# Optimization experiments

Hardware: AMD Instinct MI355X
Metric: run time of the kernel (lower is better)

The kernel has to match this reference:

```python
import jax, jax.numpy as jnp
import numpy as np

NUM_GROUPS = 4
KERNEL_SIZE = 3


def _conv1x1(x, w, b):
    # x: [B,Cin,H,W], w: [Cout,Cin], b: [Cout]
    return jnp.einsum('bchw,oc->bohw', x, w) + b[None, :, None, None]


def _unfold(t, ks):
    # t: [B,G,Gd,H,W] -> patches [B,G,Gd,ks*ks,H,W] with zero padding (pad=ks//2)
    pad = ks // 2
    H, W = t.shape[-2:]
    tp = jnp.pad(t, ((0, 0), (0, 0), (0, 0), (pad, pad), (pad, pad)))
    return jnp.stack([tp[..., i:i + H, j:j + W]
                      for i in range(ks) for j in range(ks)], axis=3)


def setup_inputs() -> dict:
    key = jax.random.key(0)
    ks = jax.random.split(key, 7)
    B, Cin, C, H, W = 4, 256, 256, 64, 64
    s = 1.0 / np.sqrt(Cin)
    return {
        'x': jax.random.normal(ks[0], (B, Cin, H, W), dtype=jnp.float32),
        'wq': jax.random.normal(ks[1], (C, Cin), dtype=jnp.float32) * s,
        'bq': jax.random.normal(ks[2], (C,), dtype=jnp.float32) * 0.01,
        'wk': jax.random.normal(ks[3], (C, Cin), dtype=jnp.float32) * s,
        'bk': jax.random.normal(ks[4], (C,), dtype=jnp.float32) * 0.01,
        'wv': jax.random.normal(ks[5], (C, Cin), dtype=jnp.float32) * s,
        'bv': jax.random.normal(ks[6], (C,), dtype=jnp.float32) * 0.01,
    }


def reference(x, wq, bq, wk, bk, wv, bv):
    B, _, H, W = x.shape
    C = wq.shape[0]
    G = NUM_GROUPS
    Gd = C // G
    q = _conv1x1(x, wq, bq).reshape(B, G, Gd, H, W)
    k = _conv1x1(x, wk, bk).reshape(B, G, Gd, H, W)
    v = _conv1x1(x, wv, bv).reshape(B, G, Gd, H, W)
    kp = _unfold(k, KERNEL_SIZE)  # [B,G,Gd,k2,H,W]
    vp = _unfold(v, KERNEL_SIZE)  # [B,G,Gd,k2,H,W]
    attn = jnp.einsum('bgdhw,bgdphw->bgphw', q, kp)  # [B,G,k2,H,W]
    attn = jax.nn.softmax(attn, axis=2)
    out = jnp.einsum('bgphw,bgdphw->bgdhw', attn, vp)  # [B,G,Gd,H,W]
    return out.reshape(B, C, H, W)
```

## Files before the change

kernel.cpp:

```cpp
#include <hip/hip_runtime.h>
#include <cstddef>
#include <cstdint>

#define BDIM 4
#define HH   64
#define WW   64
#define NG   4
#define GD   64
#define HWSZ 4096
#define NTOT 16384
#define CIN  256

typedef __attribute__((ext_vector_type(4))) float f32x4;
typedef _Float16 f16x4_t __attribute__((ext_vector_type(4)));
typedef _Float16 f16x8_t __attribute__((ext_vector_type(8)));

__device__ __forceinline__ void lds_load16(const void* g, void* l) {
    __builtin_amdgcn_global_load_lds(
        (const __attribute__((address_space(1))) unsigned int*)g,
        (__attribute__((address_space(3))) unsigned int*)l, 16, 0, 0);
}

__global__ __launch_bounds__(256) void qkv_gemm_kernel(
    const float* __restrict__ x,
    const float* __restrict__ wq, const float* __restrict__ bq,
    const float* __restrict__ wk, const float* __restrict__ bk,
    const float* __restrict__ wv, const float* __restrict__ bv,
    _Float16* __restrict__ qh, _Float16* __restrict__ kh,
    _Float16* __restrict__ vh)
{
    __shared__ float As[128 * 32];
    __shared__ float Bs[32 * 128];

    const int t  = threadIdx.x;
    const int bx = blockIdx.x;
    const int u  = (bx & 7) * 96 + (bx >> 3);
    const int mt = u % 6;
    const int nt = u / 6;

    const int l     = t & 63;
    const int wid   = t >> 6;
    const int wm    = wid >> 1, wn = wid & 1;
    const int lrow  = l & 15;
    const int grp   = l >> 4;
    const int lk8   = grp * 8;
    const int lrow4 = grp * 4;

    const float* wsel = (mt < 2) ? wq : (mt < 4) ? wk : wv;
    const float* bsel = (mt < 2) ? bq : (mt < 4) ? bk : bv;
    _Float16*    osel = (mt < 2) ? qh : (mt < 4) ? kh : vh;
    const int    mtl  = mt & 1;

    const int bi  = nt >> 5;
    const int px0 = (nt & 31) * 128;
    const float* xb = x + (size_t)bi * CIN * HWSZ + px0;

    f32x4 acc[4][4];
    #pragma unroll
    for (int mi = 0; mi < 4; ++mi) {
        const f32x4 bb = *(const f32x4*)&bsel[mtl * 128 + wm * 64 + mi * 16 + lrow4];
        #pragma unroll
        for (int ni = 0; ni < 4; ++ni) acc[mi][ni] = bb;
    }

    const float* asrc[4];
    const float* bsrc[4];
    #pragma unroll
    for (int i = 0; i < 4; ++i) {
        const int w16 = i * 256 + t;
        {
            const int m  = w16 >> 3;
            const int kb = w16 & 7;
            asrc[i] = wsel + (size_t)(mtl * 128 + m) * CIN + ((kb ^ (m & 7)) * 4);
        }
        {
            const int k   = w16 >> 5;
            const int pxb = w16 & 31;
            bsrc[i] = xb + (size_t)k * HWSZ + ((pxb ^ ((k >> 3) << 2)) * 4);
        }
    }

    for (int kt = 0; kt < 8; ++kt) {
        #pragma unroll
        for (int i = 0; i < 4; ++i) {
            lds_load16(asrc[i] + kt * 32, As + (i * 256 + t) * 4);
            lds_load16(bsrc[i] + (size_t)kt * 32 * HWSZ, Bs + (i * 256 + t) * 4);
        }
        __syncthreads();

        f16x8_t af[4];
        #pragma unroll
        for (int mi = 0; mi < 4; ++mi) {
            const int m  = wm * 64 + mi * 16 + lrow;
            const int s  = m & 7;
            const f32x4 a0 = *(const f32x4*)&As[m * 32 + ((grp * 2) ^ s) * 4];
            const f32x4 a1 = *(const f32x4*)&As[m * 32 + ((grp * 2 + 1) ^ s) * 4];
            f16x8_t f;
            #pragma unroll
            for (int j = 0; j < 4; ++j) { f[j] = (_Float16)a0[j]; f[4 + j] = (_Float16)a1[j]; }
            af[mi] = f;
        }

        f16x8_t bf[4];
        #pragma unroll
        for (int ni = 0; ni < 4; ++ni) {
            const int px   = wn * 64 + ni * 16 + lrow;
            const int base = ((px >> 2) ^ (grp << 2)) * 4 + (px & 3);
            f16x8_t f;
            #pragma unroll
            for (int j = 0; j < 8; ++j) f[j] = (_Float16)Bs[(lk8 + j) * 128 + base];
            bf[ni] = f;
        }

        #pragma unroll
        for (int mi = 0; mi < 4; ++mi)
            #pragma unroll
            for (int ni = 0; ni < 4; ++ni)
                acc[mi][ni] = __builtin_amdgcn_mfma_f32_16x16x32_f16(
                    af[mi], bf[ni], acc[mi][ni], 0, 0, 0);
        __syncthreads();
    }

    #pragma unroll
    for (int ni = 0; ni < 4; ++ni) {
        const size_t ng = (size_t)(nt * 128 + wn * 64 + ni * 16 + lrow);
        #pragma unroll
        for (int mi = 0; mi < 4; ++mi) {
            f16x4_t hv;
            #pragma unroll
            for (int j = 0; j < 4; ++j) hv[j] = (_Float16)acc[mi][ni][j];
            const int chunk = mtl * 8 + wm * 4 + mi;
            *(f16x4_t*)&osel[((size_t)chunk * NTOT + ng) * 16 + lrow4] = hv;
        }
    }
}

__global__ __launch_bounds__(256) void loc_attn_kernel(
    const _Float16* __restrict__ qh, const _Float16* __restrict__ kh,
    const _Float16* __restrict__ vh, float* __restrict__ out)
{
    const int t   = threadIdx.x;
    const int bx0 = blockIdx.x;
    const int bx  = (bx0 & 7) * 128 + (bx0 >> 3);
    const int h = bx & 63;
    const int g = (bx >> 6) & 3;
    const int b = bx >> 8;

    const int wl  = t & 15;
    const int c   = (t >> 4) & 3;
    const int wid = t >> 6;
    const int w   = wid * 16 + wl;

    const int ck = g * 4 + c;
    const size_t n = (size_t)b * HWSZ + h * 64 + w;

    float qf[16];
    {
        const _Float16* qp = &qh[((size_t)ck * NTOT + n) * 16];
        const f16x8_t q0 = *(const f16x8_t*)qp;
        const f16x8_t q1 = *(const f16x8_t*)(qp + 8);
        #pragma unroll
        for (int j = 0; j < 8; ++j) { qf[j] = (float)q0[j]; qf[8 + j] = (float)q1[j]; }
    }

    float logit[9];
    #pragma unroll
    for (int p = 0; p < 9; ++p) {
        const int dh = p / 3 - 1, dw = p % 3 - 1;
        const int hh = h + dh, ww2 = w + dw;
        float part = 0.f;
        if (hh >= 0 && hh < HH && ww2 >= 0 && ww2 < WW) {
            const size_t nn = (size_t)b * HWSZ + hh * 64 + ww2;
            const _Float16* kp = &kh[((size_t)ck * NTOT + nn) * 16];
            const f16x8_t k0 = *(const f16x8_t*)kp;
            const f16x8_t k1 = *(const f16x8_t*)(kp + 8);
            #pragma unroll
            for (int j = 0; j < 8; ++j)
                part += qf[j] * (float)k0[j] + qf[8 + j] * (float)k1[j];
        }
        part += __shfl_xor(part, 16, 64);
        part += __shfl_xor(part, 32, 64);
        logit[p] = part;
    }

    float mx = logit[0];
    #pragma unroll
    for (int p = 1; p < 9; ++p) mx = fmaxf(mx, logit[p]);
    float a[9];
    float s = 0.f;
    #pragma unroll
    for (int p = 0; p < 9; ++p) { a[p] = __expf(logit[p] - mx); s += a[p]; }
    const float inv = 1.f / s;
    #pragma unroll
    for (int p = 0; p < 9; ++p) a[p] *= inv;

    float acc[16];
    #pragma unroll
    for (int dd = 0; dd < 16; ++dd) acc[dd] = 0.f;
    #pragma unroll
    for (int p = 0; p < 9; ++p) {
        const int dh = p / 3 - 1, dw = p % 3 - 1;
        const int hh = h + dh, ww2 = w + dw;
        if (hh < 0 || hh >= HH || ww2 < 0 || ww2 >= WW) continue;
        const size_t nn = (size_t)b * HWSZ + hh * 64 + ww2;
        const _Float16* vp = &vh[((size_t)ck * NTOT + nn) * 16];
        const f16x8_t v0 = *(const f16x8_t*)vp;
        const f16x8_t v1 = *(const f16x8_t*)(vp + 8);
        const float ap = a[p];
        #pragma unroll
        for (int j = 0; j < 8; ++j) {
            acc[j]     += ap * (float)v0[j];
            acc[8 + j] += ap * (float)v1[j];
        }
    }

    const int obase = b * 256 + g * 64 + c * 16;
    const int off = h * 64 + w;
    #pragma unroll
    for (int dd = 0; dd < 16; ++dd)
        out[(size_t)(obase + dd) * HWSZ + off] = acc[dd];
}

extern "C" void kernel_launch(void* const* d_in, const int* in_sizes, int n_in,
                              void* d_out, int out_size, void* d_ws, size_t ws_size,
                              hipStream_t stream) {
    const float* x  = (const float*)d_in[0];
    const float* wq = (const float*)d_in[1];
    const float* bq = (const float*)d_in[2];
    const float* wk = (const float*)d_in[3];
    const float* bk = (const float*)d_in[4];
    const float* wv = (const float*)d_in[5];
    const float* bv = (const float*)d_in[6];
    float* out = (float*)d_out;

    char* ws = (char*)d_ws;
    _Float16* qh = (_Float16*)ws;
    _Float16* kh = (_Float16*)(ws + 8388608);
    _Float16* vh = (_Float16*)(ws + 16777216);

    qkv_gemm_kernel<<<dim3(768), 256, 0, stream>>>(x, wq, bq, wk, bk, wv, bv,
                                                   qh, kh, vh);
    loc_attn_kernel<<<dim3(1024), 256, 0, stream>>>(qh, kh, vh, out);
}
```

Measured before the change: 34.07 us.

## Fuse QKV projection and local attention into one kernel with halo recompute

Replaces the two-kernel pipeline (QKV GEMM writing fp16 workspace, then local attention reading it) with a single kernel per (batch, group, 4-row tile). Each block computes Q and K for its rows plus a one-row halo into LDS, runs the softmax, then computes V into LDS and accumulates the output. This removes the workspace round trip through global memory and one launch. In exchange it recomputes the halo rows (6 rows computed for 4 output rows), uses only 256 blocks of 512 threads, and needs large LDS, which may limit occupancy and parallelism.

```diff
diff --git a/kernel.cpp b/kernel.cpp
--- a/kernel.cpp
+++ b/kernel.cpp
@@ -5,10 +5,7 @@
 #define BDIM 4
 #define HH   64
 #define WW   64
-#define NG   4
-#define GD   64
 #define HWSZ 4096
-#define NTOT 16384
 #define CIN  256
 
 typedef __attribute__((ext_vector_type(4))) float f32x4;
@@ -21,204 +18,254 @@
         (__attribute__((address_space(3))) unsigned int*)l, 16, 0, 0);
 }
 
-__global__ __launch_bounds__(256) void qkv_gemm_kernel(
+__global__ __launch_bounds__(512, 2) void fused_kernel(
     const float* __restrict__ x,
     const float* __restrict__ wq, const float* __restrict__ bq,
     const float* __restrict__ wk, const float* __restrict__ bk,
     const float* __restrict__ wv, const float* __restrict__ bv,
-    _Float16* __restrict__ qh, _Float16* __restrict__ kh,
-    _Float16* __restrict__ vh)
+    float* __restrict__ out)
 {
-    __shared__ float As[128 * 32];
-    __shared__ float Bs[32 * 128];
-
-    const int t  = threadIdx.x;
-    const int bx = blockIdx.x;
-    const int u  = (bx & 7) * 96 + (bx >> 3);
-    const int mt = u % 6;
-    const int nt = u / 6;
-
-    const int l     = t & 63;
-    const int wid   = t >> 6;
-    const int wm    = wid >> 1, wn = wid & 1;
-    const int lrow  = l & 15;
-    const int grp   = l >> 4;
-    const int lk8   = grp * 8;
-    const int lrow4 = grp * 4;
-
-    const float* wsel = (mt < 2) ? wq : (mt < 4) ? wk : wv;
-    const float* bsel = (mt < 2) ? bq : (mt < 4) ? bk : bv;
-    _Float16*    osel = (mt < 2) ? qh : (mt < 4) ? kh : vh;
-    const int    mtl  = mt & 1;
-
-    const int bi  = nt >> 5;
-    const int px0 = (nt & 31) * 128;
-    const float* xb = x + (size_t)bi * CIN * HWSZ + px0;
-
-    f32x4 acc[4][4];
+    __shared__ float    As[128 * 32];
+    __shared__ float    Bs[32 * 384];
+    __shared__ _Float16 qlds[256 * 64];
+    __shared__ _Float16 klds[384 * 64];
+
+    const int t   = threadIdx.x;
+    const int bx0 = blockIdx.x;
+    const int bx  = (bx0 & 7) * 32 + (bx0 >> 3);
+    const int g   = bx & 3;
+    const int ht  = (bx >> 2) & 15;
+    const int b   = bx >> 6;
+    const int h0  = ht * 4;
+
+    const int l    = t & 63;
+    const int wid  = t >> 6;
+    const int lrow = l & 15;
+    const int grp  = l >> 4;
+    const int grp4 = grp * 4;
+    const int wmA  = wid >> 2;
+    const int wnA  = wid & 3;
+
+    const float* xb = x + (size_t)b * CIN * HWSZ;
+
+    const int ms  = t >> 3;
+    const int kbs = ((t & 7) ^ (ms & 7)) * 4;
+    const float* aSrcQ = wq + (size_t)(g * 64 + ms) * CIN + kbs;
+    const float* aSrcK = wk + (size_t)(g * 64 + ms) * CIN + kbs;
+    const float* aSrcV = wv + (size_t)(g * 64 + ms) * CIN + kbs;
+
+    const float* bSrc[6];
+    #pragma unroll
+    for (int i = 0; i < 6; ++i) {
+        const unsigned U = i * 512 + t;
+        const unsigned k = U / 96u;
+        const unsigned rem = U - k * 96u;
+        const int r  = (int)(rem >> 4);
+        const int u0 = (int)(rem & 15);
+        int srow = h0 - 1 + r;
+        srow = srow < 0 ? 0 : (srow > 63 ? 63 : srow);
+        const int cu = u0 ^ (((int)(k >> 3)) << 2);
+        bSrc[i] = xb + (size_t)k * HWSZ + srow * 64 + cu * 4;
+    }
+
+    const float* biasA = wmA ? bk : bq;
+    f32x4 accA[4][6];
     #pragma unroll
     for (int mi = 0; mi < 4; ++mi) {
-        const f32x4 bb = *(const f32x4*)&bsel[mtl * 128 + wm * 64 + mi * 16 + lrow4];
-        #pragma unroll
-        for (int ni = 0; ni < 4; ++ni) acc[mi][ni] = bb;
-    }
-
-    const float* asrc[4];
-    const float* bsrc[4];
-    #pragma unroll
-    for (int i = 0; i < 4; ++i) {
-        const int w16 = i * 256 + t;
-        {
-            const int m  = w16 >> 3;
-            const int kb = w16 & 7;
-            asrc[i] = wsel + (size_t)(mtl * 128 + m) * CIN + ((kb ^ (m & 7)) * 4);
-        }
-        {
-            const int k   = w16 >> 5;
-            const int pxb = w16 & 31;
-            bsrc[i] = xb + (size_t)k * HWSZ + ((pxb ^ ((k >> 3) << 2)) * 4);
-        }
+        const f32x4 bb = *(const f32x4*)&biasA[g * 64 + mi * 16 + grp4];
+        #pragma unroll
+        for (int ni = 0; ni < 6; ++ni) accA[mi][ni] = bb;
     }
 
     for (int kt = 0; kt < 8; ++kt) {
-        #pragma unroll
-        for (int i = 0; i < 4; ++i) {
-            lds_load16(asrc[i] + kt * 32, As + (i * 256 + t) * 4);
-            lds_load16(bsrc[i] + (size_t)kt * 32 * HWSZ, Bs + (i * 256 + t) * 4);
-        }
+        const size_t ko = (size_t)kt * 32;
+        lds_load16(aSrcQ + ko, As + t * 4);
+        lds_load16(aSrcK + ko, As + 2048 + t * 4);
+        #pragma unroll
+        for (int i = 0; i < 6; ++i)
+            lds_load16(bSrc[i] + ko * HWSZ, Bs + (i * 512 + t) * 4);
         __syncthreads();
 
         f16x8_t af[4];
         #pragma unroll
         for (int mi = 0; mi < 4; ++mi) {
-            const int m  = wm * 64 + mi * 16 + lrow;
-            const int s  = m & 7;
-            const f32x4 a0 = *(const f32x4*)&As[m * 32 + ((grp * 2) ^ s) * 4];
-            const f32x4 a1 = *(const f32x4*)&As[m * 32 + ((grp * 2 + 1) ^ s) * 4];
+            const int m = wmA * 64 + mi * 16 + lrow;
+            const int s = m & 7;
+            const f32x4 a0 = *(const f32x4*)&As[m * 32 + ((2 * grp) ^ s) * 4];
+            const f32x4 a1 = *(const f32x4*)&As[m * 32 + ((2 * grp + 1) ^ s) * 4];
             f16x8_t f;
             #pragma unroll
             for (int j = 0; j < 4; ++j) { f[j] = (_Float16)a0[j]; f[4 + j] = (_Float16)a1[j]; }
             af[mi] = f;
         }
-
-        f16x8_t bf[4];
-        #pragma unroll
-        for (int ni = 0; ni < 4; ++ni) {
-            const int px   = wn * 64 + ni * 16 + lrow;
-            const int base = ((px >> 2) ^ (grp << 2)) * 4 + (px & 3);
-            f16x8_t f;
-            #pragma unroll
-            for (int j = 0; j < 8; ++j) f[j] = (_Float16)Bs[(lk8 + j) * 128 + base];
+        f16x8_t bf[6];
+        #pragma unroll
+        for (int ni = 0; ni < 6; ++ni) {
+            const int px  = wnA * 96 + ni * 16 + lrow;
+            const int fo  = ((px >> 2) ^ (grp << 2)) * 4 + (px & 3);
+            f16x8_t f;
+            #pragma unroll
+            for (int j = 0; j < 8; ++j) f[j] = (_Float16)Bs[(grp * 8 + j) * 384 + fo];
             bf[ni] = f;
         }
-
         #pragma unroll
         for (int mi = 0; mi < 4; ++mi)
             #pragma unroll
-            for (int ni = 0; ni < 4; ++ni)
-                acc[mi][ni] = __builtin_amdgcn_mfma_f32_16x16x32_f16(
-                    af[mi], bf[ni], acc[mi][ni], 0, 0, 0);
-        __syncthreads();
-    }
-
-    #pragma unroll
-    for (int ni = 0; ni < 4; ++ni) {
-        const size_t ng = (size_t)(nt * 128 + wn * 64 + ni * 16 + lrow);
-        #pragma unroll
-        for (int mi = 0; mi < 4; ++mi) {
-            f16x4_t hv;
-            #pragma unroll
-            for (int j = 0; j < 4; ++j) hv[j] = (_Float16)acc[mi][ni][j];
-            const int chunk = mtl * 8 + wm * 4 + mi;
-            *(f16x4_t*)&osel[((size_t)chunk * NTOT + ng) * 16 + lrow4] = hv;
-        }
-    }
-}
-
-__global__ __launch_bounds__(256) void loc_attn_kernel(
-    const _Float16* __restrict__ qh, const _Float16* __restrict__ kh,
-    const _Float16* __restrict__ vh, float* __restrict__ out)
-{
-    const int t   = threadIdx.x;
-    const int bx0 = blockIdx.x;
-    const int bx  = (bx0 & 7) * 128 + (bx0 >> 3);
-    const int h = bx & 63;
-    const int g = (bx >> 6) & 3;
-    const int b = bx >> 8;
-
-    const int wl  = t & 15;
-    const int c   = (t >> 4) & 3;
-    const int wid = t >> 6;
-    const int w   = wid * 16 + wl;
-
-    const int ck = g * 4 + c;
-    const size_t n = (size_t)b * HWSZ + h * 64 + w;
-
-    float qf[16];
-    {
-        const _Float16* qp = &qh[((size_t)ck * NTOT + n) * 16];
-        const f16x8_t q0 = *(const f16x8_t*)qp;
-        const f16x8_t q1 = *(const f16x8_t*)(qp + 8);
-        #pragma unroll
-        for (int j = 0; j < 8; ++j) { qf[j] = (float)q0[j]; qf[8 + j] = (float)q1[j]; }
-    }
-
-    float logit[9];
+            for (int ni = 0; ni < 6; ++ni)
+                accA[mi][ni] = __builtin_amdgcn_mfma_f32_16x16x32_f16(
+                    af[mi], bf[ni], accA[mi][ni], 0, 0, 0);
+        __syncthreads();
+    }
+
+    #pragma unroll
+    for (int ni = 0; ni < 6; ++ni) {
+        const int px = wnA * 96 + ni * 16 + lrow;
+        const int spx = (wmA == 0) ? (px - 64) : px;
+        const bool ok = (wmA == 0) ? (spx >= 0 && spx < 256) : true;
+        _Float16* dl = (wmA == 0) ? qlds : klds;
+        #pragma unroll
+        for (int mi = 0; mi < 4; ++mi) {
+            if (ok) {
+                const int cb  = mi * 2 + (grp >> 1);
+                const int off = (grp & 1) * 4;
+                f16x4_t hv;
+                #pragma unroll
+                for (int j = 0; j < 4; ++j) hv[j] = (_Float16)accA[mi][ni][j];
+                *(f16x4_t*)&dl[spx * 64 + ((cb ^ (spx & 7)) * 8) + off] = hv;
+            }
+        }
+    }
+    __syncthreads();
+
+    const int pxi  = wid * 32 + (l & 31);
+    const int chh  = l >> 5;
+    const int hq   = h0 + (pxi >> 6);
+    const int wcol = pxi & 63;
+
+    float qf[32];
+    #pragma unroll
+    for (int jj = 0; jj < 4; ++jj) {
+        const int cb = chh * 4 + jj;
+        const f16x8_t qv = *(const f16x8_t*)&qlds[pxi * 64 + ((cb ^ (pxi & 7)) * 8)];
+        #pragma unroll
+        for (int e = 0; e < 8; ++e) qf[jj * 8 + e] = (float)qv[e];
+    }
+
+    float lg[9];
     #pragma unroll
     for (int p = 0; p < 9; ++p) {
         const int dh = p / 3 - 1, dw = p % 3 - 1;
-        const int hh = h + dh, ww2 = w + dw;
+        const int h2 = hq + dh, w2 = wcol + dw;
         float part = 0.f;
-        if (hh >= 0 && hh < HH && ww2 >= 0 && ww2 < WW) {
-            const size_t nn = (size_t)b * HWSZ + hh * 64 + ww2;
-            const _Float16* kp = &kh[((size_t)ck * NTOT + nn) * 16];
-            const f16x8_t k0 = *(const f16x8_t*)kp;
-            const f16x8_t k1 = *(const f16x8_t*)(kp + 8);
-            #pragma unroll
-            for (int j = 0; j < 8; ++j)
-                part += qf[j] * (float)k0[j] + qf[8 + j] * (float)k1[j];
-        }
-        part += __shfl_xor(part, 16, 64);
+        if (h2 >= 0 && h2 < HH && w2 >= 0 && w2 < WW) {
+            const int hpx = pxi + 64 + dh * 64 + dw;
+            #pragma unroll
+            for (int jj = 0; jj < 4; ++jj) {
+                const int cb = chh * 4 + jj;
+                const f16x8_t kv = *(const f16x8_t*)&klds[hpx * 64 + ((cb ^ (hpx & 7)) * 8)];
+                #pragma unroll
+                for (int e = 0; e < 8; ++e) part += qf[jj * 8 + e] * (float)kv[e];
+            }
+        }
         part += __shfl_xor(part, 32, 64);
-        logit[p] = part;
-    }
-
-    float mx = logit[0];
-    #pragma unroll
-    for (int p = 1; p < 9; ++p) mx = fmaxf(mx, logit[p]);
+        lg[p] = part;
+    }
+
+    float mx = lg[0];
+    #pragma unroll
+    for (int p = 1; p < 9; ++p) mx = fmaxf(mx, lg[p]);
     float a[9];
-    float s = 0.f;
-    #pragma unroll
-    for (int p = 0; p < 9; ++p) { a[p] = __expf(logit[p] - mx); s += a[p]; }
-    const float inv = 1.f / s;
+    float sum = 0.f;
+    #pragma unroll
+    for (int p = 0; p < 9; ++p) { a[p] = __expf(lg[p] - mx); sum += a[p]; }
+    const float inv = 1.f / sum;
     #pragma unroll
     for (int p = 0; p < 9; ++p) a[p] *= inv;
 
-    float acc[16];
-    #pragma unroll
-    for (int dd = 0; dd < 16; ++dd) acc[dd] = 0.f;
+    f32x4 accB[4][3];
+    #pragma unroll
+    for (int mi = 0; mi < 4; ++mi) {
+        const f32x4 bb = *(const f32x4*)&bv[g * 64 + mi * 16 + grp4];
+        #pragma unroll
+        for (int ni = 0; ni < 3; ++ni) accB[mi][ni] = bb;
+    }
+
+    for (int kt = 0; kt < 8; ++kt) {
+        const size_t ko = (size_t)kt * 32;
+        lds_load16(aSrcV + ko, As + t * 4);
+        #pragma unroll
+        for (int i = 0; i < 6; ++i)
+            lds_load16(bSrc[i] + ko * HWSZ, Bs + (i * 512 + t) * 4);
+        __syncthreads();
+
+        f16x8_t af[4];
+        #pragma unroll
+        for (int mi = 0; mi < 4; ++mi) {
+            const int m = mi * 16 + lrow;
+            const int s = m & 7;
+            const f32x4 a0 = *(const f32x4*)&As[m * 32 + ((2 * grp) ^ s) * 4];
+            const f32x4 a1 = *(const f32x4*)&As[m * 32 + ((2 * grp + 1) ^ s) * 4];
+            f16x8_t f;
+            #pragma unroll
+            for (int j = 0; j < 4; ++j) { f[j] = (_Float16)a0[j]; f[4 + j] = (_Float16)a1[j]; }
+            af[mi] = f;
+        }
+        f16x8_t bf[3];
+        #pragma unroll
+        for (int ni = 0; ni < 3; ++ni) {
+            const int px = wid * 48 + ni * 16 + lrow;
+            const int fo = ((px >> 2) ^ (grp << 2)) * 4 + (px & 3);
+            f16x8_t f;
+            #pragma unroll
+            for (int j = 0; j < 8; ++j) f[j] = (_Float16)Bs[(grp * 8 + j) * 384 + fo];
+            bf[ni] = f;
+        }
+        #pragma unroll
+        for (int mi = 0; mi < 4; ++mi)
+            #pragma unroll
+            for (int ni = 0; ni < 3; ++ni)
+                accB[mi][ni] = __builtin_amdgcn_mfma_f32_16x16x32_f16(
+                    af[mi], bf[ni], accB[mi][ni], 0, 0, 0);
+        __syncthreads();
+    }
+
+    #pragma unroll
+    for (int ni = 0; ni < 3; ++ni) {
+        const int px = wid * 48 + ni * 16 + lrow;
+        #pragma unroll
+        for (int mi = 0; mi < 4; ++mi) {
+            const int cb  = mi * 2 + (grp >> 1);
+            const int off = (grp & 1) * 4;
+            f16x4_t hv;
+            #pragma unroll
+            for (int j = 0; j < 4; ++j) hv[j] = (_Float16)accB[mi][ni][j];
+            *(f16x4_t*)&klds[px * 64 + ((cb ^ (px & 7)) * 8) + off] = hv;
+        }
+    }
+    __syncthreads();
+
+    float oacc[32];
+    #pragma unroll
+    for (int c = 0; c < 32; ++c) oacc[c] = 0.f;
     #pragma unroll
     for (int p = 0; p < 9; ++p) {
         const int dh = p / 3 - 1, dw = p % 3 - 1;
-        const int hh = h + dh, ww2 = w + dw;
-        if (hh < 0 || hh >= HH || ww2 < 0 || ww2 >= WW) continue;
-        const size_t nn = (size_t)b * HWSZ + hh * 64 + ww2;
-        const _Float16* vp = &vh[((size_t)ck * NTOT + nn) * 16];
-        const f16x8_t v0 = *(const f16x8_t*)vp;
-        const f16x8_t v1 = *(const f16x8_t*)(vp + 8);
+        const int h2 = hq + dh, w2 = wcol + dw;
+        if (h2 < 0 || h2 >= HH || w2 < 0 || w2 >= WW) continue;
         const float ap = a[p];
-        #pragma unroll
-        for (int j = 0; j < 8; ++j) {
-            acc[j]     += ap * (float)v0[j];
-            acc[8 + j] += ap * (float)v1[j];
-        }
-    }
-
-    const int obase = b * 256 + g * 64 + c * 16;
-    const int off = h * 64 + w;
-    #pragma unroll
-    for (int dd = 0; dd < 16; ++dd)
-        out[(size_t)(obase + dd) * HWSZ + off] = acc[dd];
+        const int hpx = pxi + 64 + dh * 64 + dw;
+        #pragma unroll
+        for (int jj = 0; jj < 4; ++jj) {
+            const int cb = chh * 4 + jj;
+            const f16x8_t vv = *(const f16x8_t*)&klds[hpx * 64 + ((cb ^ (hpx & 7)) * 8)];
+            #pragma unroll
+            for (int e = 0; e < 8; ++e) oacc[jj * 8 + e] += ap * (float)vv[e];
+        }
+    }
+
+    float* ob = out + ((size_t)(b * 256 + g * 64 + chh * 32)) * HWSZ + ht * 256 + pxi;
+    #pragma unroll
+    for (int c = 0; c < 32; ++c) ob[(size_t)c * HWSZ] = oacc[c];
 }
 
 extern "C" void kernel_launch(void* const* d_in, const int* in_sizes, int n_in,
@@ -233,12 +280,5 @@
     const float* bv = (const float*)d_in[6];
     float* out = (float*)d_out;
 
-    char* ws = (char*)d_ws;
-    _Float16* qh = (_Float16*)ws;
-    _Float16* kh = (_Float16*)(ws + 8388608);
-    _Float16* vh = (_Float16*)(ws + 16777216);
-
-    qkv_gemm_kernel<<<dim3(768), 256, 0, stream>>>(x, wq, bq, wk, bk, wv, bv,
-                                                   qh, kh, vh);
-    loc_attn_kernel<<<dim3(1024), 256, 0, stream>>>(qh, kh, vh, out);
+    fused_kernel<<<dim3(256), 512, 0, stream>>>(x, wq, bq, wk, bk, wv, bv, out);
 }
```

New measurement: 37.54 us. 10.2% more time.

## Double-buffer QKV GEMM tiles and pre-convert x to fp16 transposed in LDS

Applied to the files above, without the earlier changes.

Adds double-buffered LDS tiles to the QKV GEMM, so the next K-slice of weights is prefetched asynchronously while MFMAs run on the current slice. The x tile is no longer copied straight to LDS. It is loaded into registers, converted to fp16 and stored transposed with a swizzle, so each B fragment becomes a single 16-byte LDS read instead of eight scalar reads plus conversions. It also sets a minimum of 3 blocks per CU in the launch bounds. The costs are more LDS per block, more register pressure from the prefetch registers, and strided per-thread global loads of x.

```diff
diff --git a/kernel.cpp b/kernel.cpp
--- a/kernel.cpp
+++ b/kernel.cpp
@@ -21,7 +21,7 @@
         (__attribute__((address_space(3))) unsigned int*)l, 16, 0, 0);
 }
 
-__global__ __launch_bounds__(256) void qkv_gemm_kernel(
+__global__ __launch_bounds__(256, 3) void qkv_gemm_kernel(
     const float* __restrict__ x,
     const float* __restrict__ wq, const float* __restrict__ bq,
     const float* __restrict__ wk, const float* __restrict__ bk,
@@ -29,8 +29,8 @@
     _Float16* __restrict__ qh, _Float16* __restrict__ kh,
     _Float16* __restrict__ vh)
 {
-    __shared__ float As[128 * 32];
-    __shared__ float Bs[32 * 128];
+    __shared__ float    As[2][128 * 32];
+    __shared__ _Float16 Bs[2][128 * 32];
 
     const int t  = threadIdx.x;
     const int bx = blockIdx.x;
@@ -43,7 +43,6 @@
     const int wm    = wid >> 1, wn = wid & 1;
     const int lrow  = l & 15;
     const int grp   = l >> 4;
-    const int lk8   = grp * 8;
     const int lrow4 = grp * 4;
 
     const float* wsel = (mt < 2) ? wq : (mt < 4) ? wk : wv;
@@ -53,7 +52,6 @@
 
     const int bi  = nt >> 5;
     const int px0 = (nt & 31) * 128;
-    const float* xb = x + (size_t)bi * CIN * HWSZ + px0;
 
     f32x4 acc[4][4];
     #pragma unroll
@@ -64,60 +62,84 @@
     }
 
     const float* asrc[4];
-    const float* bsrc[4];
     #pragma unroll
     for (int i = 0; i < 4; ++i) {
         const int w16 = i * 256 + t;
-        {
-            const int m  = w16 >> 3;
-            const int kb = w16 & 7;
-            asrc[i] = wsel + (size_t)(mtl * 128 + m) * CIN + ((kb ^ (m & 7)) * 4);
-        }
-        {
-            const int k   = w16 >> 5;
-            const int pxb = w16 & 31;
-            bsrc[i] = xb + (size_t)k * HWSZ + ((pxb ^ ((k >> 3) << 2)) * 4);
-        }
+        const int m  = w16 >> 3;
+        const int kb = w16 & 7;
+        asrc[i] = wsel + (size_t)(mtl * 128 + m) * CIN + ((kb ^ (m & 7)) * 4);
+    }
+
+    const int spx  = t & 127;
+    const int sko0 = t >> 7;
+    const float* xbp = x + (size_t)bi * CIN * HWSZ + px0 + spx;
+    const int bw0 = spx * 32 + ((sko0       ^ (spx & 3)) * 8);
+    const int bw1 = spx * 32 + (((sko0 + 2) ^ (spx & 3)) * 8);
+
+    {
+        #pragma unroll
+        for (int i = 0; i < 4; ++i)
+            lds_load16(asrc[i], &As[0][(i * 256 + t) * 4]);
+        float r0[8], r1[8];
+        #pragma unroll
+        for (int j = 0; j < 8; ++j) r0[j] = xbp[(size_t)(sko0 * 8 + j) * HWSZ];
+        #pragma unroll
+        for (int j = 0; j < 8; ++j) r1[j] = xbp[(size_t)((sko0 + 2) * 8 + j) * HWSZ];
+        f16x8_t w0, w1;
+        #pragma unroll
+        for (int j = 0; j < 8; ++j) { w0[j] = (_Float16)r0[j]; w1[j] = (_Float16)r1[j]; }
+        *(f16x8_t*)&Bs[0][bw0] = w0;
+        *(f16x8_t*)&Bs[0][bw1] = w1;
+        __syncthreads();
     }
 
     for (int kt = 0; kt < 8; ++kt) {
-        #pragma unroll
-        for (int i = 0; i < 4; ++i) {
-            lds_load16(asrc[i] + kt * 32, As + (i * 256 + t) * 4);
-            lds_load16(bsrc[i] + (size_t)kt * 32 * HWSZ, Bs + (i * 256 + t) * 4);
-        }
-        __syncthreads();
+        const int cur = kt & 1, nxt = cur ^ 1;
+
+        float r0[8], r1[8];
+        if (kt < 7) {
+            const int kb = (kt + 1) * 32;
+            #pragma unroll
+            for (int i = 0; i < 4; ++i)
+                lds_load16(asrc[i] + kb, &As[nxt][(i * 256 + t) * 4]);
+            #pragma unroll
+            for (int j = 0; j < 8; ++j) r0[j] = xbp[(size_t)(kb + sko0 * 8 + j) * HWSZ];
+            #pragma unroll
+            for (int j = 0; j < 8; ++j) r1[j] = xbp[(size_t)(kb + (sko0 + 2) * 8 + j) * HWSZ];
+        }
 
         f16x8_t af[4];
         #pragma unroll
         for (int mi = 0; mi < 4; ++mi) {
-            const int m  = wm * 64 + mi * 16 + lrow;
-            const int s  = m & 7;
-            const f32x4 a0 = *(const f32x4*)&As[m * 32 + ((grp * 2) ^ s) * 4];
-            const f32x4 a1 = *(const f32x4*)&As[m * 32 + ((grp * 2 + 1) ^ s) * 4];
+            const int m = wm * 64 + mi * 16 + lrow;
+            const int s = m & 7;
+            const f32x4 a0 = *(const f32x4*)&As[cur][m * 32 + ((2 * grp) ^ s) * 4];
+            const f32x4 a1 = *(const f32x4*)&As[cur][m * 32 + ((2 * grp + 1) ^ s) * 4];
             f16x8_t f;
             #pragma unroll
             for (int j = 0; j < 4; ++j) { f[j] = (_Float16)a0[j]; f[4 + j] = (_Float16)a1[j]; }
             af[mi] = f;
         }
-
         f16x8_t bf[4];
         #pragma unroll
         for (int ni = 0; ni < 4; ++ni) {
-            const int px   = wn * 64 + ni * 16 + lrow;
-            const int base = ((px >> 2) ^ (grp << 2)) * 4 + (px & 3);
-            f16x8_t f;
-            #pragma unroll
-            for (int j = 0; j < 8; ++j) f[j] = (_Float16)Bs[(lk8 + j) * 128 + base];
-            bf[ni] = f;
-        }
-
+            const int px = wn * 64 + ni * 16 + lrow;
+            bf[ni] = *(const f16x8_t*)&Bs[cur][px * 32 + ((grp ^ (px & 3)) * 8)];
+        }
         #pragma unroll
         for (int mi = 0; mi < 4; ++mi)
             #pragma unroll
             for (int ni = 0; ni < 4; ++ni)
                 acc[mi][ni] = __builtin_amdgcn_mfma_f32_16x16x32_f16(
                     af[mi], bf[ni], acc[mi][ni], 0, 0, 0);
+
+        if (kt < 7) {
+            f16x8_t w0, w1;
+            #pragma unroll
+            for (int j = 0; j < 8; ++j) { w0[j] = (_Float16)r0[j]; w1[j] = (_Float16)r1[j]; }
+            *(f16x8_t*)&Bs[nxt][bw0] = w0;
+            *(f16x8_t*)&Bs[nxt][bw1] = w1;
+        }
         __syncthreads();
     }
 
```

New measurement: 33.71 us (median of 2 runs). No clear change (-1.0%).
